# Optimization experiments

Hardware: AMD Instinct MI355X
Metric: run time of the kernel (lower is better)

The kernel has to match this reference:

```python
import jax, jax.numpy as jnp
import numpy as np
from jax import lax

EPS = 1e-20  # matches sample_gumbel eps in the TF source


def setup_inputs() -> dict:
    key = jax.random.key(0)
    ks = jax.random.split(key, 7)
    B, T, D, H, K = 32, 512, 512, 512, 64
    x = jax.random.normal(ks[0], (B, T, D), jnp.float32)
    f_after = jax.random.normal(ks[1], (K, D, H), jnp.float32) * 0.02
    f_skip = jax.random.normal(ks[2], (2 * H, 2), jnp.float32) * 0.05
    gru_kernel = jax.random.normal(ks[3], (D, 3 * H), jnp.float32) * 0.02
    gru_rec_kernel = jax.random.normal(ks[4], (H, 3 * H), jnp.float32) * 0.02
    gru_bias = jnp.zeros((2, 3 * H), jnp.float32)
    u_gumbel = jax.random.uniform(ks[5], (T, B, 2), jnp.float32)
    return {"x": x, "f_after": f_after, "f_skip": f_skip,
            "gru_kernel": gru_kernel, "gru_rec_kernel": gru_rec_kernel,
            "gru_bias": gru_bias, "u_gumbel": u_gumbel}


def reference(x, f_after, f_skip, gru_kernel, gru_rec_kernel, gru_bias, u_gumbel):
    # z_after = tanh(conv1d(x, f_after, SAME))  -> [B, T, H]
    z_after = lax.conv_general_dilated(
        x, f_after, window_strides=(1,), padding='SAME',
        dimension_numbers=('NWC', 'WIO', 'NWC'))
    z_after = jnp.tanh(z_after)

    # gumbel(0,1) noise from uniform draws, per step: [T, B, 2]
    g = -jnp.log(-jnp.log(u_gumbel + EPS) + EPS)

    b_in, b_rec = gru_bias[0], gru_bias[1]  # reset_after=True biases, each [3H]
    H = gru_rec_kernel.shape[0]
    B = x.shape[0]
    h0 = jnp.zeros((B, H), x.dtype)

    xs = (jnp.swapaxes(x, 0, 1), jnp.swapaxes(z_after, 0, 1), g)  # time-major

    def step(h_prev, inp):
        x_t, za_t, g_t = inp
        # skip gate: concat(h_{t-1}, z_after_t) @ f_skip, gumbel-softmax (temp=1)
        logits = jnp.concatenate([h_prev, za_t], axis=-1) @ f_skip  # [B, 2]
        skip = jax.nn.softmax(logits + g_t, axis=-1)
        # Keras GRUCell (reset_after=True), gate order z, r, h
        xm = x_t @ gru_kernel + b_in          # [B, 3H]
        hm = h_prev @ gru_rec_kernel + b_rec  # [B, 3H]
        xz, xr, xh = jnp.split(xm, 3, axis=-1)
        hz, hr, hh = jnp.split(hm, 3, axis=-1)
        z = jax.nn.sigmoid(xz + hz)
        r = jax.nn.sigmoid(xr + hr)
        hc = jnp.tanh(xh + r * hh)
        ht = z * h_prev + (1.0 - z) * hc
        # skip blend
        ht = skip[:, 0:1] * h_prev + skip[:, 1:2] * ht
        return ht, ht

    _, ys = lax.scan(step, h0, xs)           # [T, B, H]
    return jnp.swapaxes(ys, 0, 1)            # [B, T, H]
```

## Files before the change

### kernel.cpp

```cpp
#include <hip/hip_runtime.h>
#include <stdint.h>

typedef unsigned short u16;
typedef unsigned int   u32;
typedef __attribute__((ext_vector_type(8))) short short8;
typedef __attribute__((ext_vector_type(4))) float f32x4;
typedef __attribute__((ext_vector_type(4))) u32   u32x4;

#define AS1 __attribute__((address_space(1)))
#define AS3 __attribute__((address_space(3)))

#define SENT 0x7FC0u

__device__ __forceinline__ float bf2f(u16 u) {
  union { u32 i; float f; } v; v.i = ((u32)u) << 16; return v.f;
}
__device__ __forceinline__ u16 f2bf(float f) {
  union { float f; u32 i; } v; v.f = f;
  u32 i = v.i;
  i += 0x7FFFu + ((i >> 16) & 1u);
  return (u16)(i >> 16);
}

__device__ __forceinline__ void gload16(const u16* src, u16* ldsDst) {
  __builtin_amdgcn_global_load_lds((const AS1 u32*)src, (AS3 u32*)ldsDst, 16, 0, 0);
}

__device__ __forceinline__ short8 ldg_sc_h_wait(const u16* p) {
  short8 r;
  asm volatile("global_load_dwordx4 %0, %1, off sc0 sc1\n\t"
               "s_waitcnt vmcnt(0)"
               : "=v"(r) : "v"(p) : "memory");
  return r;
}
__device__ __forceinline__ void stg_sc_h(u16* p, u16 v) {
  asm volatile("global_store_short %0, %1, off sc0 sc1" :: "v"(p), "v"((u32)v) : "memory");
}

__global__ void k_init(const float* __restrict__ x, u16* __restrict__ xp) {
  const long NXP = 32L * 576 * 512;
  long i0 = (long)blockIdx.x * 256 + threadIdx.x;
  for (long i = i0; i < NXP; i += (long)gridDim.x * 256) {
    long b = i / (576 * 512);
    int rem = (int)(i - b * (576 * 512));
    int rr = rem >> 9, dd = rem & 511;
    int t = rr - 31;
    float v = (t >= 0 && t < 512) ? x[(b * 512 + t) * 512 + dd] : 0.f;
    xp[i] = f2bf(v);
  }
}

__global__ void k_sent(u32* __restrict__ hs) {
  const u32x4 s = u32x4{(SENT << 16) | SENT, (SENT << 16) | SENT,
                        (SENT << 16) | SENT, (SENT << 16) | SENT};
  *(u32x4*)&hs[((long)blockIdx.x * 256 + threadIdx.x) * 4] = s;
}

__global__ void k_transpose_cast(const float* __restrict__ in, u16* __restrict__ out,
                                 int rows, int cols, long inWStride, long outWStride) {
  __shared__ float tile[64][65];
  const int w = blockIdx.z;
  const float* ip = in + (long)w * inWStride;
  u16* op = out + (long)w * outWStride;
  const int r0 = blockIdx.y * 64, c0 = blockIdx.x * 64;
  const int tr = threadIdx.x >> 6, tc = threadIdx.x & 63;
  #pragma unroll
  for (int p = 0; p < 16; ++p) {
    int rr = p * 4 + tr;
    tile[rr][tc] = ip[(long)(r0 + rr) * cols + c0 + tc];
  }
  __syncthreads();
  #pragma unroll
  for (int p = 0; p < 16; ++p) {
    int rr = p * 4 + tr;
    op[(long)(c0 + rr) * rows + r0 + tc] = f2bf(tile[tc][rr]);
  }
}

__global__ __launch_bounds__(256) void k_gemm(
    const u16* __restrict__ A, const u16* __restrict__ Bm, u16* __restrict__ C,
    int nTiles, int kw, int woff, long bWStride, int outMode)
{
  __shared__ __align__(16) u16 Alds[128 * 64];
  __shared__ __align__(16) u16 Blds[128 * 64];
  const int bid = blockIdx.x;
  const int mt = bid / nTiles, nt = bid - mt * nTiles;
  const int bb = (mt * 128) >> 9;
  const int t0 = (mt * 128) & 511;
  const int h0 = nt * 128;
  const int tid = threadIdx.x;
  const int wv = tid >> 6, l = tid & 63;
  const int wr = wv >> 1, wc = wv & 1;
  const int sRow = wv * 8 + (l >> 3);
  const int sCol = (l & 7) * 8;
  f32x4 acc[4][4];
  #pragma unroll
  for (int m = 0; m < 4; ++m)
    #pragma unroll
    for (int n = 0; n < 4; ++n) acc[m][n] = f32x4{0.f, 0.f, 0.f, 0.f};

  const int kIters = kw * 8;
  const long aRow0 = (long)(bb * 576 + t0 + woff);
  for (int q = 0; q < kIters; ++q) {
    const int w = q >> 3, dsub = (q & 7) << 6;
    const u16* aB = A + (aRow0 + w) * 512 + dsub + sCol;
    const u16* bB = Bm + (long)w * bWStride + (long)h0 * 512 + dsub + sCol;
    __syncthreads();
    #pragma unroll
    for (int c = 0; c < 4; ++c) {
      gload16(aB + (long)(c * 32 + sRow) * 512, &Alds[c * 2048 + wv * 512]);
      gload16(bB + (long)(c * 32 + sRow) * 512, &Blds[c * 2048 + wv * 512]);
    }
    __syncthreads();
    #pragma unroll
    for (int kk = 0; kk < 2; ++kk) {
      short8 af[4], bf[4];
      #pragma unroll
      for (int m = 0; m < 4; ++m)
        af[m] = *(const short8*)&Alds[(wr * 64 + m * 16 + (l & 15)) * 64 + kk * 32 + (l >> 4) * 8];
      #pragma unroll
      for (int n = 0; n < 4; ++n)
        bf[n] = *(const short8*)&Blds[(wc * 64 + n * 16 + (l & 15)) * 64 + kk * 32 + (l >> 4) * 8];
      #pragma unroll
      for (int m = 0; m < 4; ++m)
        #pragma unroll
        for (int n = 0; n < 4; ++n)
          acc[m][n] = __builtin_amdgcn_mfma_f32_16x16x32_bf16(af[m], bf[n], acc[m][n], 0, 0, 0);
    }
  }
  const int lr = (l >> 4) * 4, lc = l & 15;
  #pragma unroll
  for (int m = 0; m < 4; ++m)
    #pragma unroll
    for (int n = 0; n < 4; ++n)
      #pragma unroll
      for (int r = 0; r < 4; ++r) {
        const int row = mt * 128 + wr * 64 + m * 16 + lr + r;
        const int col = h0 + wc * 64 + n * 16 + lc;
        const float v = acc[m][n][r];
        if (outMode == 0) {
          C[(long)row * 512 + col] = f2bf(tanhf(v));
        } else {
          const int b = row >> 9, t = row & 511;
          C[((long)t * 32 + b) * 1536 + col] = f2bf(v);
        }
      }
}

__global__ void k_dza(const u16* __restrict__ za, const float* __restrict__ fskip,
                      const float* __restrict__ ug, float* __restrict__ dza) {
  __shared__ float wd2[512];
  const int t = blockIdx.x, tid = threadIdx.x;
  for (int i = tid; i < 512; i += 256) wd2[i] = fskip[(512 + i) * 2 + 1] - fskip[(512 + i) * 2];
  __syncthreads();
  const int b = tid >> 3, seg = (tid & 7) * 64;
  const u16* row = za + ((long)b * 512 + t) * 512 + seg;
  float pp = 0.f;
  #pragma unroll
  for (int j = 0; j < 8; ++j) {
    short8 v = *(const short8*)&row[j * 8];
    #pragma unroll
    for (int e = 0; e < 8; ++e) pp += bf2f((u16)v[e]) * wd2[seg + j * 8 + e];
  }
  pp += __shfl_xor(pp, 1); pp += __shfl_xor(pp, 2); pp += __shfl_xor(pp, 4);
  if ((tid & 7) == 0) {
    float u0 = ug[((long)t * 32 + b) * 2 + 0], u1 = ug[((long)t * 32 + b) * 2 + 1];
    float g0 = -logf(-logf(u0 + 1e-20f) + 1e-20f);
    float g1 = -logf(-logf(u1 + 1e-20f) + 1e-20f);
    dza[t * 32 + b] = pp + (g1 - g0);
  }
}

__global__ __launch_bounds__(256, 1) void k_rnn(
    const u16* __restrict__ XM, const float* __restrict__ dza,
    const float* __restrict__ Wrec, const float* __restrict__ gbias,
    const float* __restrict__ fskip, u16* hstep, float* __restrict__ out)
{
  const int bid = blockIdx.x, d = bid & 7, s = bid >> 3;
  const int tid = threadIdx.x, wv = tid >> 6, l = tid & 63;
  __shared__ __align__(16) u16 hBl[2][2048];
  __shared__ float s1s[2][4];

  float wdv[8];
  #pragma unroll
  for (int e = 0; e < 8; ++e)
    wdv[e] = fskip[(l * 8 + e) * 2 + 1] - fskip[(l * 8 + e) * 2];

  const int colb = s * 64 + wv * 16 + (l & 15);
  short8 wf[3][16];
  #pragma unroll
  for (int g = 0; g < 3; ++g)
    #pragma unroll
    for (int kk = 0; kk < 16; ++kk) {
      short8 tmp;
      #pragma unroll
      for (int e = 0; e < 8; ++e)
        tmp[e] = (short)f2bf(Wrec[(long)(kk * 32 + (l >> 4) * 8 + e) * 1536 + g * 512 + colb]);
      wf[g][kk] = tmp;
    }
  float bi[3], br[3];
  #pragma unroll
  for (int g = 0; g < 3; ++g) {
    bi[g] = gbias[g * 512 + colb];
    br[g] = gbias[1536 + g * 512 + colb];
  }
  const int myb = d * 4;
  float hp[4] = {0.f, 0.f, 0.f, 0.f};

  for (int t = 0; t < 512; ++t) {
    const int p = t & 1;
    u16 xmv[3][4];
    if (l < 16) {
      const u16* xr = XM + ((long)t * 32 + myb) * 1536;
      #pragma unroll
      for (int r = 0; r < 4; ++r)
        #pragma unroll
        for (int g = 0; g < 3; ++g)
          xmv[g][r] = xr[(long)r * 1536 + g * 512 + colb];
    }
    const float dzv = dza[t * 32 + myb + wv];

    short8 h8;
    if (t > 0) {
      const u16* ph = hstep + ((long)(t - 1) * 32 + myb + wv) * 512 + l * 8;
      h8 = ldg_sc_h_wait(ph);
      bool bad = true;
      while (bad) {
        bad = false;
        #pragma unroll
        for (int e = 0; e < 8; ++e) bad |= ((u16)h8[e] == SENT);
        if (bad) h8 = ldg_sc_h_wait(ph);
      }
    } else {
      #pragma unroll
      for (int e = 0; e < 8; ++e) h8[e] = 0;
    }

    float pp = 0.f;
    #pragma unroll
    for (int e = 0; e < 8; ++e) pp += bf2f((u16)h8[e]) * wdv[e];
    #pragma unroll
    for (int o = 1; o < 64; o <<= 1) pp += __shfl_xor(pp, o);
    if (l == 0) s1s[p][wv] = 1.f / (1.f + __expf(-(pp + dzv)));
    *(short8*)&hBl[p][tid * 8] = h8;
    __syncthreads();

    f32x4 acc[3];
    acc[0] = f32x4{0.f, 0.f, 0.f, 0.f}; acc[1] = acc[0]; acc[2] = acc[0];
    const int b4 = l & 3;
    #pragma unroll
    for (int kk = 0; kk < 16; ++kk) {
      short8 a = *(const short8*)&hBl[p][b4 * 512 + kk * 32 + (l >> 4) * 8];
      acc[0] = __builtin_amdgcn_mfma_f32_16x16x32_bf16(a, wf[0][kk], acc[0], 0, 0, 0);
      acc[1] = __builtin_amdgcn_mfma_f32_16x16x32_bf16(a, wf[1][kk], acc[1], 0, 0, 0);
      acc[2] = __builtin_amdgcn_mfma_f32_16x16x32_bf16(a, wf[2][kk], acc[2], 0, 0, 0);
    }
    if (l < 16) {
      #pragma unroll
      for (int r = 0; r < 4; ++r) {
        const float xz = bf2f(xmv[0][r]) + bi[0];
        const float xr_ = bf2f(xmv[1][r]) + bi[1];
        const float xh = bf2f(xmv[2][r]) + bi[2];
        const float hz = acc[0][r] + br[0];
        const float hr = acc[1][r] + br[1];
        const float hh = acc[2][r] + br[2];
        const float z  = 1.f / (1.f + __expf(-(xz + hz)));
        const float rr = 1.f / (1.f + __expf(-(xr_ + hr)));
        const float hc = tanhf(xh + rr * hh);
        const float ht = z * hp[r] + (1.f - z) * hc;
        const float s1 = s1s[p][r];
        const float hn = hp[r] + s1 * (ht - hp[r]);
        stg_sc_h(&hstep[((long)t * 32 + myb + r) * 512 + colb], f2bf(hn));
        hp[r] = hn;
      }
      #pragma unroll
      for (int r = 0; r < 4; ++r)
        out[((long)(myb + r) * 512 + t) * 512 + colb] = hp[r];
    }
    asm volatile("s_waitcnt vmcnt(0)" ::: "memory");
  }
}

extern "C" void kernel_launch(void* const* d_in, const int* in_sizes, int n_in,
                              void* d_out, int out_size, void* d_ws, size_t ws_size,
                              hipStream_t stream) {
  (void)in_sizes; (void)n_in; (void)out_size; (void)ws_size;
  const float* x        = (const float*)d_in[0];
  const float* f_after  = (const float*)d_in[1];
  const float* f_skip   = (const float*)d_in[2];
  const float* gru_k    = (const float*)d_in[3];
  const float* gru_rec  = (const float*)d_in[4];
  const float* gru_bias = (const float*)d_in[5];
  const float* ug       = (const float*)d_in[6];
  float* out = (float*)d_out;

  char* ws = (char*)d_ws;
  size_t off = 0;
  auto alloc = [&](size_t bytes) { void* p = ws + off; off = (off + bytes + 255) & ~(size_t)255; return p; };
  u16*  xp    = (u16*)alloc(32L * 576 * 512 * 2);
  u16*  fT    = (u16*)alloc(64L * 512 * 512 * 2);
  u16*  gruT  = (u16*)alloc(1536L * 512 * 2);
  u16*  za    = (u16*)alloc(32L * 512 * 512 * 2);
  u16*  XM    = (u16*)alloc(512L * 32 * 1536 * 2);
  float* dza  = (float*)alloc(512L * 32 * 4);
  u16*  hstep = za;

  k_init<<<dim3(4096), dim3(256), 0, stream>>>(x, xp);
  k_transpose_cast<<<dim3(8, 8, 64), dim3(256), 0, stream>>>(f_after, fT, 512, 512, 512L * 512, 512L * 512);
  k_transpose_cast<<<dim3(24, 8, 1), dim3(256), 0, stream>>>(gru_k, gruT, 512, 1536, 0L, 0L);
  k_gemm<<<dim3(512), dim3(256), 0, stream>>>(xp, fT, za, 4, 64, 0, 512L * 512, 0);
  k_gemm<<<dim3(1536), dim3(256), 0, stream>>>(xp, gruT, XM, 12, 1, 31, 0L, 1);
  k_dza<<<dim3(512), dim3(256), 0, stream>>>(za, f_skip, ug, dza);
  k_sent<<<dim3(4096), dim3(256), 0, stream>>>((u32*)hstep);
  k_rnn<<<dim3(64), dim3(256), 0, stream>>>(XM, dza, gru_rec, gru_bias, f_skip, hstep, out);
}
```

Before: 2.207 ms.

## Fold skip-gate dot into MFMA, prefetch next-step inputs, use fast tanh

The skip-gate logit is now computed as a fourth MFMA against a bf16 column of f_skip differences. This replaces the per-wave shuffle reduction and the LDS broadcast of the skip probability. The x-projection and dza values for step t+1 are loaded during step t, which hides their latency on the serial recurrence. tanhf is replaced with an exp-based approximation, and the trailing vmcnt(0) wait is dropped. The costs are extra registers for the wdf fragments, bf16 rounding of the skip weights, and reliance on the wait inside the h-load asm to order memory.

```diff
diff --git a/kernel.cpp b/kernel.cpp
--- a/kernel.cpp
+++ b/kernel.cpp
@@ -20,6 +20,11 @@
   u32 i = v.i;
   i += 0x7FFFu + ((i >> 16) & 1u);
   return (u16)(i >> 16);
+}
+__device__ __forceinline__ float tanh_fast(float x) {
+  const float e = __expf(-2.f * fabsf(x));
+  const float t = (1.f - e) / (1.f + e);
+  return __builtin_copysignf(t, x);
 }
 
 __device__ __forceinline__ void gload16(const u16* src, u16* ldsDst) {
@@ -179,14 +184,10 @@
   const int bid = blockIdx.x, d = bid & 7, s = bid >> 3;
   const int tid = threadIdx.x, wv = tid >> 6, l = tid & 63;
   __shared__ __align__(16) u16 hBl[2][2048];
-  __shared__ float s1s[2][4];
-
-  float wdv[8];
-  #pragma unroll
-  for (int e = 0; e < 8; ++e)
-    wdv[e] = fskip[(l * 8 + e) * 2 + 1] - fskip[(l * 8 + e) * 2];
 
   const int colb = s * 64 + wv * 16 + (l & 15);
+  const int kq = (l >> 4) * 8;
+
   short8 wf[3][16];
   #pragma unroll
   for (int g = 0; g < 3; ++g)
@@ -195,9 +196,20 @@
       short8 tmp;
       #pragma unroll
       for (int e = 0; e < 8; ++e)
-        tmp[e] = (short)f2bf(Wrec[(long)(kk * 32 + (l >> 4) * 8 + e) * 1536 + g * 512 + colb]);
+        tmp[e] = (short)f2bf(Wrec[(long)(kk * 32 + kq + e) * 1536 + g * 512 + colb]);
       wf[g][kk] = tmp;
     }
+  short8 wdf[16];
+  #pragma unroll
+  for (int kk = 0; kk < 16; ++kk) {
+    short8 tmp;
+    #pragma unroll
+    for (int e = 0; e < 8; ++e) {
+      const int k = kk * 32 + kq + e;
+      tmp[e] = (short)f2bf(fskip[k * 2 + 1] - fskip[k * 2]);
+    }
+    wdf[kk] = tmp;
+  }
   float bi[3], br[3];
   #pragma unroll
   for (int g = 0; g < 3; ++g) {
@@ -207,18 +219,19 @@
   const int myb = d * 4;
   float hp[4] = {0.f, 0.f, 0.f, 0.f};
 
+  u16 xmc[3][4]; f32x4 dzc;
+  if (l < 16) {
+    const u16* xr = XM + (long)myb * 1536;
+    #pragma unroll
+    for (int r = 0; r < 4; ++r)
+      #pragma unroll
+      for (int g = 0; g < 3; ++g)
+        xmc[g][r] = xr[(long)r * 1536 + g * 512 + colb];
+    dzc = *(const f32x4*)&dza[myb];
+  }
+
   for (int t = 0; t < 512; ++t) {
     const int p = t & 1;
-    u16 xmv[3][4];
-    if (l < 16) {
-      const u16* xr = XM + ((long)t * 32 + myb) * 1536;
-      #pragma unroll
-      for (int r = 0; r < 4; ++r)
-        #pragma unroll
-        for (int g = 0; g < 3; ++g)
-          xmv[g][r] = xr[(long)r * 1536 + g * 512 + colb];
-    }
-    const float dzv = dza[t * 32 + myb + wv];
 
     short8 h8;
     if (t > 0) {
@@ -236,39 +249,48 @@
       for (int e = 0; e < 8; ++e) h8[e] = 0;
     }
 
-    float pp = 0.f;
-    #pragma unroll
-    for (int e = 0; e < 8; ++e) pp += bf2f((u16)h8[e]) * wdv[e];
-    #pragma unroll
-    for (int o = 1; o < 64; o <<= 1) pp += __shfl_xor(pp, o);
-    if (l == 0) s1s[p][wv] = 1.f / (1.f + __expf(-(pp + dzv)));
+    u16 xmn[3][4]; f32x4 dzn;
+    const int tn = (t < 511) ? t + 1 : t;
+    if (l < 16) {
+      const u16* xr = XM + ((long)tn * 32 + myb) * 1536;
+      #pragma unroll
+      for (int r = 0; r < 4; ++r)
+        #pragma unroll
+        for (int g = 0; g < 3; ++g)
+          xmn[g][r] = xr[(long)r * 1536 + g * 512 + colb];
+      dzn = *(const f32x4*)&dza[tn * 32 + myb];
+    }
+
     *(short8*)&hBl[p][tid * 8] = h8;
     __syncthreads();
 
-    f32x4 acc[3];
-    acc[0] = f32x4{0.f, 0.f, 0.f, 0.f}; acc[1] = acc[0]; acc[2] = acc[0];
+    f32x4 acc[4];
+    acc[0] = f32x4{0.f, 0.f, 0.f, 0.f};
+    acc[1] = acc[0]; acc[2] = acc[0]; acc[3] = acc[0];
     const int b4 = l & 3;
     #pragma unroll
     for (int kk = 0; kk < 16; ++kk) {
-      short8 a = *(const short8*)&hBl[p][b4 * 512 + kk * 32 + (l >> 4) * 8];
+      short8 a = *(const short8*)&hBl[p][b4 * 512 + kk * 32 + kq];
       acc[0] = __builtin_amdgcn_mfma_f32_16x16x32_bf16(a, wf[0][kk], acc[0], 0, 0, 0);
       acc[1] = __builtin_amdgcn_mfma_f32_16x16x32_bf16(a, wf[1][kk], acc[1], 0, 0, 0);
       acc[2] = __builtin_amdgcn_mfma_f32_16x16x32_bf16(a, wf[2][kk], acc[2], 0, 0, 0);
-    }
+      acc[3] = __builtin_amdgcn_mfma_f32_16x16x32_bf16(a, wdf[kk],  acc[3], 0, 0, 0);
+    }
+
     if (l < 16) {
       #pragma unroll
       for (int r = 0; r < 4; ++r) {
-        const float xz = bf2f(xmv[0][r]) + bi[0];
-        const float xr_ = bf2f(xmv[1][r]) + bi[1];
-        const float xh = bf2f(xmv[2][r]) + bi[2];
+        const float xz = bf2f(xmc[0][r]) + bi[0];
+        const float xr_ = bf2f(xmc[1][r]) + bi[1];
+        const float xh = bf2f(xmc[2][r]) + bi[2];
         const float hz = acc[0][r] + br[0];
         const float hr = acc[1][r] + br[1];
         const float hh = acc[2][r] + br[2];
         const float z  = 1.f / (1.f + __expf(-(xz + hz)));
         const float rr = 1.f / (1.f + __expf(-(xr_ + hr)));
-        const float hc = tanhf(xh + rr * hh);
+        const float hc = tanh_fast(xh + rr * hh);
         const float ht = z * hp[r] + (1.f - z) * hc;
-        const float s1 = s1s[p][r];
+        const float s1 = 1.f / (1.f + __expf(-(acc[3][r] + dzc[r])));
         const float hn = hp[r] + s1 * (ht - hp[r]);
         stg_sc_h(&hstep[((long)t * 32 + myb + r) * 512 + colb], f2bf(hn));
         hp[r] = hn;
@@ -276,8 +298,12 @@
       #pragma unroll
       for (int r = 0; r < 4; ++r)
         out[((long)(myb + r) * 512 + t) * 512 + colb] = hp[r];
-    }
-    asm volatile("s_waitcnt vmcnt(0)" ::: "memory");
+      #pragma unroll
+      for (int g = 0; g < 3; ++g)
+        #pragma unroll
+        for (int r = 0; r < 4; ++r) xmc[g][r] = xmn[g][r];
+      dzc = dzn;
+    }
   }
 }
 
```

New measurement: 2.333 ms. 5.7% more time.
